# Optimization experiments

Hardware: AMD Instinct MI355X
Metric: run time of the kernel (lower is better)

## Reference

```python
import jax, jax.numpy as jnp
import numpy as np

N = 40000      # nodes
E = 640000     # edges (avg degree 16)
F = 128        # in_feats
OUT = 128      # out_feats


def setup_inputs() -> dict:
    key = jax.random.key(0)
    ks = jax.random.split(key, 8)
    feat = jax.random.normal(ks[0], (N, F), dtype=jnp.float32)
    src = jax.random.randint(ks[1], (E,), 0, N, dtype=jnp.int32)
    dst = jnp.sort(jax.random.randint(ks[2], (E,), 0, N, dtype=jnp.int32))
    # AttentionAGG: fc1 (2F -> F), fc2 (F -> 1); fc_layer (2F -> OUT)
    s1 = 1.0 / np.sqrt(2 * F)
    s2 = 1.0 / np.sqrt(F)
    w1 = jax.random.normal(ks[3], (2 * F, F), dtype=jnp.float32) * s1
    b1 = jnp.zeros((F,), dtype=jnp.float32)
    w2 = jax.random.normal(ks[4], (F, 1), dtype=jnp.float32) * s2
    b2 = jnp.zeros((1,), dtype=jnp.float32)
    wf = jax.random.normal(ks[5], (2 * F, OUT), dtype=jnp.float32) * s1
    bf = jnp.zeros((OUT,), dtype=jnp.float32)
    return {"feat": feat, "src": src, "dst": dst,
            "w1": w1, "b1": b1, "w2": w2, "b2": b2, "wf": wf, "bf": bf}


def reference(feat, src, dst, w1, b1, w2, b2, wf, bf):
    f = feat.shape[1]
    n = feat.shape[0]
    # fc1(concat(h_dst, m_src)) == h_dst @ w1[:F] + h_src @ w1[F:]  (edge_weight is None)
    proj_dst = feat @ w1[:f]          # [N, F]
    proj_src = feat @ w1[f:]          # [N, F]
    pre = jnp.tanh(proj_dst[dst] + proj_src[src] + b1)   # [E, F]
    scores = (pre @ w2)[:, 0] + b2[0]                    # [E]
    # softmax over the ragged incoming-edge set of each dst node
    smax = jax.ops.segment_max(scores, dst, num_segments=n, indices_are_sorted=True)
    ex = jnp.exp(scores - jax.lax.stop_gradient(smax)[dst])
    den = jax.ops.segment_sum(ex, dst, num_segments=n, indices_are_sorted=True)
    att = ex / den[dst]                                  # [E]
    # weighted segment-sum of messages (m_e = feat[src]); zero-degree nodes get 0
    neigh = jax.ops.segment_sum(att[:, None] * feat[src], dst,
                                num_segments=n, indices_are_sorted=True)  # [N, F]
    # fc_layer(concat(h_self, neigh))
    rst = feat @ wf[:f] + neigh @ wf[f:] + bf            # [N, OUT]
    return rst
```

## Files before the change

### kernel.cpp

```cpp
#include <hip/hip_runtime.h>
#include <math.h>

#define F 128
#define OUT 128

typedef unsigned short ushort_t;
typedef __attribute__((ext_vector_type(8))) short bfrag;
typedef __attribute__((ext_vector_type(4))) float ffrag;

union BU { unsigned u[4]; bfrag b; };

__device__ __forceinline__ float bf_lo(unsigned int u) {
    return __uint_as_float(u << 16);
}
__device__ __forceinline__ float bf_hi(unsigned int u) {
    return __uint_as_float(u & 0xffff0000u);
}
__device__ __forceinline__ ushort_t f2bf(float f) {
    unsigned int x = __float_as_uint(f);
    unsigned int r = x + 0x7fffu + ((x >> 16) & 1u);
    return (ushort_t)(r >> 16);
}
__device__ __forceinline__ unsigned pk2(float lo, float hi) {
    return (unsigned)f2bf(lo) | ((unsigned)f2bf(hi) << 16);
}

#define PSTRIDE 136
__global__ __launch_bounds__(256) void mega_kernel(
    const float* __restrict__ feat, const float* __restrict__ w1,
    const float* __restrict__ b1, const int* __restrict__ dst,
    int* __restrict__ row_ptr, ushort_t* __restrict__ e_dst,
    ushort_t* __restrict__ srcpack, ushort_t* __restrict__ abig,
    int n, int e, int nproj)
{
    if ((int)blockIdx.x >= nproj) {
        int i = ((int)blockIdx.x - nproj) * 256 + threadIdx.x;
        if (i >= e) return;
        int d = dst[i];
        int prev = (i == 0) ? -1 : dst[i - 1];
        for (int v = prev + 1; v <= d; ++v) row_ptr[v] = i;
        if (i == e - 1) {
            for (int v = d + 1; v <= n; ++v) row_ptr[v] = e;
        }
        return;
    }

    __shared__ ushort_t As[64 * PSTRIDE];
    const int t = threadIdx.x;
    const int wv = t >> 6, lane = t & 63;
    const int lm = lane & 15, quad = lane >> 4;
    const int row0 = blockIdx.x * 64;
    const int col0 = wv * 64;

    {
        const int r = t >> 2, q = t & 3;
        const int row = row0 + r;
        unsigned up[16];
        if (row < n) {
            const float* fp = feat + (size_t)row * F + 32 * q;
#pragma unroll
            for (int i4 = 0; i4 < 8; ++i4) {
                float4 a = *(const float4*)(fp + 4 * i4);
                up[2 * i4]     = pk2(a.x, a.y);
                up[2 * i4 + 1] = pk2(a.z, a.w);
            }
        } else {
#pragma unroll
            for (int i2 = 0; i2 < 16; ++i2) up[i2] = 0;
        }
#pragma unroll
        for (int i4 = 0; i4 < 4; ++i4)
            *(uint4*)(As + r * PSTRIDE + 32 * q + 8 * i4) =
                make_uint4(up[4 * i4], up[4 * i4 + 1], up[4 * i4 + 2], up[4 * i4 + 3]);
        if (row < n) {
#pragma unroll
            for (int i4 = 0; i4 < 4; ++i4)
                *(uint4*)(abig + (size_t)row * 256 + 32 * q + 8 * i4) =
                    make_uint4(up[4 * i4], up[4 * i4 + 1], up[4 * i4 + 2], up[4 * i4 + 3]);
#pragma unroll
            for (int i4 = 0; i4 < 8; ++i4)
                *(uint2*)(srcpack + (size_t)row * 256 + (8 * q + i4) * 8 + 4) =
                    make_uint2(up[2 * i4], up[2 * i4 + 1]);
        }
    }
    __syncthreads();

    ffrag acc[4][4];
#pragma unroll
    for (int mi = 0; mi < 4; ++mi)
#pragma unroll
        for (int ni = 0; ni < 4; ++ni) acc[mi][ni] = (ffrag){0.f, 0.f, 0.f, 0.f};

#pragma unroll
    for (int ks = 0; ks < 4; ++ks) {
        bfrag bfr[4];
#pragma unroll
        for (int ni = 0; ni < 4; ++ni) {
            const int jj = col0 + ni * 16 + lm;
            const float* wcol = (jj < F) ? (w1 + jj) : (w1 + (size_t)F * F + (jj - F));
            const int k0 = ks * 32 + quad * 8;
            BU bu;
#pragma unroll
            for (int l = 0; l < 4; ++l) {
                float x0 = wcol[(size_t)(k0 + 2 * l) * F];
                float x1 = wcol[(size_t)(k0 + 2 * l + 1) * F];
                bu.u[l] = pk2(x0, x1);
            }
            bfr[ni] = bu.b;
        }
#pragma unroll
        for (int mi = 0; mi < 4; ++mi) {
            bfrag af = *(const bfrag*)(As + (mi * 16 + lm) * PSTRIDE
                                       + ks * 32 + quad * 8);
#pragma unroll
            for (int ni = 0; ni < 4; ++ni)
                acc[mi][ni] = __builtin_amdgcn_mfma_f32_16x16x32_bf16(
                    af, bfr[ni], acc[mi][ni], 0, 0, 0);
        }
    }

#pragma unroll
    for (int ni = 0; ni < 4; ++ni) {
        const int j = col0 + ni * 16 + lm;
        const float bias = (j < F) ? b1[j] : 0.f;
#pragma unroll
        for (int mi = 0; mi < 4; ++mi) {
#pragma unroll
            for (int r = 0; r < 4; ++r) {
                int row = row0 + mi * 16 + quad * 4 + r;
                if (row >= n) continue;
                ushort_t ub = f2bf(__expf(2.f * (acc[mi][ni][r] + bias)));
                if (j < F) {
                    e_dst[(size_t)row * F + j] = ub;
                } else {
                    int f = j - F;
                    srcpack[(size_t)row * 256 + (f >> 2) * 8 + (f & 3)] = ub;
                }
            }
        }
    }
}

__global__ __launch_bounds__(256) void fused_kernel(
    const ushort_t* __restrict__ e_dst, const ushort_t* __restrict__ srcpack,
    const int* __restrict__ src, const int* __restrict__ row_ptr,
    const float* __restrict__ w2, ushort_t* __restrict__ abig, int n)
{
    const int v = (int)((blockIdx.x * 256u + threadIdx.x) >> 5);
    const int fl = threadIdx.x & 31;
    const int sbase = threadIdx.x & 32;

    const float4 wv4 = ((const float4*)w2)[fl];
    const float w0 = wv4.x, w1_ = wv4.y, w2_ = wv4.z, w3_ = wv4.w;
    float sw = w0 + w1_ + w2_ + w3_;
    float aw = fabsf(w0) + fabsf(w1_) + fabsf(w2_) + fabsf(w3_);
#pragma unroll
    for (int off = 16; off; off >>= 1) {
        sw += __shfl_xor(sw, off, 64);
        aw += __shfl_xor(aw, off, 64);
    }
    const float K = sw - aw;

    if (v >= n) return;
    const int begin = row_ptr[v], end = row_ptr[v + 1];

    const uint2 ud = *(const uint2*)(e_dst + (size_t)v * F + fl * 4);
    const float ea0 = bf_lo(ud.x), ea1 = bf_hi(ud.x);
    const float ea2 = bf_lo(ud.y), ea3 = bf_hi(ud.y);

    float s = 0.f, a0 = 0.f, a1 = 0.f, a2 = 0.f, a3 = 0.f;

    for (int cb = begin; cb < end; cb += 32) {
        const int clen = min(32, end - cb);
        const int sv = (fl < clen) ? src[cb + fl] : 0;
        int jj = 0;
        for (; jj + 4 <= clen; jj += 4) {
            uint4 u[4];
#pragma unroll
            for (int q = 0; q < 4; ++q) {
                const int sq = __shfl(sv, sbase + jj + q, 64);
                u[q] = ((const uint4*)(srcpack + (size_t)sq * 256))[fl];
            }
            float p[4];
#pragma unroll
            for (int q = 0; q < 4; ++q) {
                float r;
                r = __builtin_amdgcn_rcpf(fmaf(ea0, bf_lo(u[q].x), 1.f)); p[q] = w0 * r;
                r = __builtin_amdgcn_rcpf(fmaf(ea1, bf_hi(u[q].x), 1.f)); p[q] = fmaf(w1_, r, p[q]);
                r = __builtin_amdgcn_rcpf(fmaf(ea2, bf_lo(u[q].y), 1.f)); p[q] = fmaf(w2_, r, p[q]);
                r = __builtin_amdgcn_rcpf(fmaf(ea3, bf_hi(u[q].y), 1.f)); p[q] = fmaf(w3_, r, p[q]);
            }
#pragma unroll
            for (int off = 16; off; off >>= 1) {
#pragma unroll
                for (int q = 0; q < 4; ++q) p[q] += __shfl_xor(p[q], off, 64);
            }
            float g[4];
#pragma unroll
            for (int q = 0; q < 4; ++q) g[q] = __expf(fmaf(-2.f, p[q], K));
            s += (g[0] + g[1]) + (g[2] + g[3]);
#pragma unroll
            for (int q = 0; q < 4; ++q) {
                a0 = fmaf(g[q], bf_lo(u[q].z), a0);
                a1 = fmaf(g[q], bf_hi(u[q].z), a1);
                a2 = fmaf(g[q], bf_lo(u[q].w), a2);
                a3 = fmaf(g[q], bf_hi(u[q].w), a3);
            }
        }
        for (; jj < clen; ++jj) {
            const int s0 = __shfl(sv, sbase + jj, 64);
            const uint4 u0 = ((const uint4*)(srcpack + (size_t)s0 * 256))[fl];
            float r, p0;
            r = __builtin_amdgcn_rcpf(fmaf(ea0, bf_lo(u0.x), 1.f)); p0 = w0 * r;
            r = __builtin_amdgcn_rcpf(fmaf(ea1, bf_hi(u0.x), 1.f)); p0 = fmaf(w1_, r, p0);
            r = __builtin_amdgcn_rcpf(fmaf(ea2, bf_lo(u0.y), 1.f)); p0 = fmaf(w2_, r, p0);
            r = __builtin_amdgcn_rcpf(fmaf(ea3, bf_hi(u0.y), 1.f)); p0 = fmaf(w3_, r, p0);
#pragma unroll
            for (int off = 16; off; off >>= 1) p0 += __shfl_xor(p0, off, 64);
            const float g0 = __expf(fmaf(-2.f, p0, K));
            s += g0;
            a0 = fmaf(g0, bf_lo(u0.z), a0);
            a1 = fmaf(g0, bf_hi(u0.z), a1);
            a2 = fmaf(g0, bf_lo(u0.w), a2);
            a3 = fmaf(g0, bf_hi(u0.w), a3);
        }
    }

    const float inv = (end > begin) ? 1.f / s : 0.f;
    ushort4 o = make_ushort4(f2bf(a0 * inv), f2bf(a1 * inv),
                             f2bf(a2 * inv), f2bf(a3 * inv));
    *(ushort4*)(abig + (size_t)v * 256 + 128 + fl * 4) = o;
}

#define OSTRIDE 264
__global__ __launch_bounds__(256) void out_mfma_kernel(
    const ushort_t* __restrict__ abig, const float* __restrict__ wf,
    const float* __restrict__ bfv, float* __restrict__ out, int n)
{
    __shared__ ushort_t As[64 * OSTRIDE];
    const int t = threadIdx.x;
    const int wv = t >> 6, lane = t & 63;
    const int lm = lane & 15, quad = lane >> 4;
    const int row0 = blockIdx.x * 64;
    const int col0 = wv * 32;

    for (int i = t; i < 2048; i += 256) {
        int r = i >> 5, c8 = (i & 31) * 8;
        uint4 d = make_uint4(0, 0, 0, 0);
        if (row0 + r < n)
            d = *(const uint4*)(abig + (size_t)(row0 + r) * 256 + c8);
        *(uint4*)(As + r * OSTRIDE + c8) = d;
    }
    __syncthreads();

    ffrag acc[4][2];
#pragma unroll
    for (int mi = 0; mi < 4; ++mi)
#pragma unroll
        for (int ni = 0; ni < 2; ++ni) acc[mi][ni] = (ffrag){0.f, 0.f, 0.f, 0.f};

#pragma unroll
    for (int ks = 0; ks < 8; ++ks) {
        bfrag bfr[2];
#pragma unroll
        for (int ni = 0; ni < 2; ++ni) {
            const int jj = col0 + ni * 16 + lm;
            const int k0 = ks * 32 + quad * 8;
            BU bu;
#pragma unroll
            for (int l = 0; l < 4; ++l) {
                float x0 = wf[(size_t)(k0 + 2 * l) * F + jj];
                float x1 = wf[(size_t)(k0 + 2 * l + 1) * F + jj];
                bu.u[l] = pk2(x0, x1);
            }
            bfr[ni] = bu.b;
        }
#pragma unroll
        for (int mi = 0; mi < 4; ++mi) {
            bfrag af = *(const bfrag*)(As + (mi * 16 + lm) * OSTRIDE
                                       + ks * 32 + quad * 8);
#pragma unroll
            for (int ni = 0; ni < 2; ++ni)
                acc[mi][ni] = __builtin_amdgcn_mfma_f32_16x16x32_bf16(
                    af, bfr[ni], acc[mi][ni], 0, 0, 0);
        }
    }

#pragma unroll
    for (int ni = 0; ni < 2; ++ni) {
        const int j = col0 + ni * 16 + lm;
        const float bb = bfv[j];
#pragma unroll
        for (int mi = 0; mi < 4; ++mi) {
#pragma unroll
            for (int r = 0; r < 4; ++r) {
                int row = row0 + mi * 16 + quad * 4 + r;
                if (row < n) out[(size_t)row * OUT + j] = acc[mi][ni][r] + bb;
            }
        }
    }
}

extern "C" void kernel_launch(void* const* d_in, const int* in_sizes, int n_in,
                              void* d_out, int out_size, void* d_ws, size_t ws_size,
                              hipStream_t stream)
{
    const float* feat = (const float*)d_in[0];
    const int*   src  = (const int*)d_in[1];
    const int*   dst  = (const int*)d_in[2];
    const float* w1   = (const float*)d_in[3];
    const float* b1   = (const float*)d_in[4];
    const float* w2   = (const float*)d_in[5];
    const float* b2   = (const float*)d_in[6];  (void)b2;
    const float* wf   = (const float*)d_in[7];
    const float* bfv  = (const float*)d_in[8];
    float* out = (float*)d_out;

    const int n = in_sizes[0] / F;
    const int e = in_sizes[1];

    ushort_t* abig    = (ushort_t*)d_ws;
    ushort_t* e_dst   = abig + (size_t)n * 256;
    ushort_t* srcpack = e_dst + (size_t)n * 128;
    int* row_ptr      = (int*)(srcpack + (size_t)n * 256);

    const int nproj = (n + 63) / 64;
    const int nrp   = (e + 255) / 256;

    mega_kernel<<<nproj + nrp, 256, 0, stream>>>(
        feat, w1, b1, dst, row_ptr, e_dst, srcpack, abig, n, e, nproj);
    fused_kernel<<<(n + 7) / 8, 256, 0, stream>>>(
        e_dst, srcpack, src, row_ptr, w2, abig, n);
    out_mfma_kernel<<<(n + 63) / 64, 256, 0, stream>>>(abig, wf, bfv, out, n);
}
```

Measured before the change: 177.7 us.

## Pre-transpose weights to bf16 once and split projection GEMM into separate prep pass

Adds a prep kernel that converts feat to bf16, builds the packed source buffer, and writes w1 and wf transposed as bf16 so GEMM kernels can load B fragments with single vector loads instead of strided fp32 gathers plus conversion in every block. The projection GEMM now reads bf16 rows from the workspace and stages its epilogue through shared memory so e_dst and srcpack are written with wide coalesced stores instead of scattered 2-byte stores. The cost is an extra kernel launch and an extra global round-trip for the bf16 feature copy, which the projection GEMM previously produced in-register.

```diff
diff --git a/kernel.cpp b/kernel.cpp
--- a/kernel.cpp
+++ b/kernel.cpp
@@ -7,8 +7,6 @@
 typedef unsigned short ushort_t;
 typedef __attribute__((ext_vector_type(8))) short bfrag;
 typedef __attribute__((ext_vector_type(4))) float ffrag;
-
-union BU { unsigned u[4]; bfrag b; };
 
 __device__ __forceinline__ float bf_lo(unsigned int u) {
     return __uint_as_float(u << 16);
@@ -25,16 +23,37 @@
     return (unsigned)f2bf(lo) | ((unsigned)f2bf(hi) << 16);
 }
 
-#define PSTRIDE 136
-__global__ __launch_bounds__(256) void mega_kernel(
+__global__ __launch_bounds__(256) void prep_kernel(
     const float* __restrict__ feat, const float* __restrict__ w1,
-    const float* __restrict__ b1, const int* __restrict__ dst,
-    int* __restrict__ row_ptr, ushort_t* __restrict__ e_dst,
-    ushort_t* __restrict__ srcpack, ushort_t* __restrict__ abig,
-    int n, int e, int nproj)
-{
-    if ((int)blockIdx.x >= nproj) {
-        int i = ((int)blockIdx.x - nproj) * 256 + threadIdx.x;
+    const float* __restrict__ wf, const int* __restrict__ dst,
+    ushort_t* __restrict__ abig, ushort_t* __restrict__ srcpack,
+    ushort_t* __restrict__ btp, ushort_t* __restrict__ btf,
+    int* __restrict__ row_ptr, int n, int e, int nb0, int nb1, int nb2)
+{
+    const int b = blockIdx.x, t = threadIdx.x;
+    if (b < nb0) {
+        int i = b * 256 + t;
+        if (i >= n * 16) return;
+        int row = i >> 4, c = (i & 15) * 8;
+        float4 a = *(const float4*)(feat + (size_t)row * F + c);
+        float4 bb = *(const float4*)(feat + (size_t)row * F + c + 4);
+        unsigned p0 = pk2(a.x, a.y), p1 = pk2(a.z, a.w);
+        unsigned p2 = pk2(bb.x, bb.y), p3 = pk2(bb.z, bb.w);
+        *(uint4*)(abig + (size_t)row * 256 + c) = make_uint4(p0, p1, p2, p3);
+        *(uint2*)(srcpack + (size_t)row * 256 + c * 2 + 4) = make_uint2(p0, p1);
+        *(uint2*)(srcpack + (size_t)row * 256 + c * 2 + 12) = make_uint2(p2, p3);
+    } else if (b < nb0 + nb1) {
+        int idx = (b - nb0) * 256 + t;
+        int j = idx >> 7, k = idx & 127;
+        float v = (j < F) ? w1[(size_t)k * F + j]
+                          : w1[(size_t)(F + k) * F + (j - F)];
+        btp[idx] = f2bf(v);
+    } else if (b < nb0 + nb1 + nb2) {
+        int idx = (b - nb0 - nb1) * 256 + t;
+        int j = idx >> 8, k = idx & 255;
+        btf[idx] = f2bf(wf[(size_t)k * F + j]);
+    } else {
+        int i = (b - nb0 - nb1 - nb2) * 256 + t;
         if (i >= e) return;
         int d = dst[i];
         int prev = (i == 0) ? -1 : dst[i - 1];
@@ -42,49 +61,40 @@
         if (i == e - 1) {
             for (int v = d + 1; v <= n; ++v) row_ptr[v] = e;
         }
-        return;
-    }
-
-    __shared__ ushort_t As[64 * PSTRIDE];
+    }
+}
+
+#define PST 136
+__global__ __launch_bounds__(256) void proj_gemm_kernel(
+    const ushort_t* __restrict__ abig, const ushort_t* __restrict__ btp,
+    const float* __restrict__ b1, ushort_t* __restrict__ e_dst,
+    ushort_t* __restrict__ srcpack, int n)
+{
+    __shared__ ushort_t As[64 * PST];
+    __shared__ ushort_t Ep[4][16 * 80];
     const int t = threadIdx.x;
     const int wv = t >> 6, lane = t & 63;
     const int lm = lane & 15, quad = lane >> 4;
-    const int row0 = blockIdx.x * 64;
-    const int col0 = wv * 64;
-
-    {
-        const int r = t >> 2, q = t & 3;
-        const int row = row0 + r;
-        unsigned up[16];
-        if (row < n) {
-            const float* fp = feat + (size_t)row * F + 32 * q;
-#pragma unroll
-            for (int i4 = 0; i4 < 8; ++i4) {
-                float4 a = *(const float4*)(fp + 4 * i4);
-                up[2 * i4]     = pk2(a.x, a.y);
-                up[2 * i4 + 1] = pk2(a.z, a.w);
-            }
-        } else {
-#pragma unroll
-            for (int i2 = 0; i2 < 16; ++i2) up[i2] = 0;
-        }
-#pragma unroll
-        for (int i4 = 0; i4 < 4; ++i4)
-            *(uint4*)(As + r * PSTRIDE + 32 * q + 8 * i4) =
-                make_uint4(up[4 * i4], up[4 * i4 + 1], up[4 * i4 + 2], up[4 * i4 + 3]);
-        if (row < n) {
-#pragma unroll
-            for (int i4 = 0; i4 < 4; ++i4)
-                *(uint4*)(abig + (size_t)row * 256 + 32 * q + 8 * i4) =
-                    make_uint4(up[4 * i4], up[4 * i4 + 1], up[4 * i4 + 2], up[4 * i4 + 3]);
-#pragma unroll
-            for (int i4 = 0; i4 < 8; ++i4)
-                *(uint2*)(srcpack + (size_t)row * 256 + (8 * q + i4) * 8 + 4) =
-                    make_uint2(up[2 * i4], up[2 * i4 + 1]);
-        }
+    const int row0 = blockIdx.x * 64, col0 = wv * 64;
+
+#pragma unroll
+    for (int k = 0; k < 4; ++k) {
+        int l = k * 256 + t;
+        int r = l >> 4, ch = l & 15;
+        uint4 d = make_uint4(0, 0, 0, 0);
+        if (row0 + r < n) d = *(const uint4*)(abig + (size_t)(row0 + r) * 256 + ch * 8);
+        *(uint4*)(As + r * PST + ch * 8) = d;
     }
     __syncthreads();
 
+    bfrag bfr[4][4];
+#pragma unroll
+    for (int ks = 0; ks < 4; ++ks)
+#pragma unroll
+        for (int ni = 0; ni < 4; ++ni)
+            bfr[ks][ni] = *(const bfrag*)(btp + (size_t)(col0 + ni * 16 + lm) * 128
+                                          + ks * 32 + quad * 8);
+
     ffrag acc[4][4];
 #pragma unroll
     for (int mi = 0; mi < 4; ++mi)
@@ -92,49 +102,43 @@
         for (int ni = 0; ni < 4; ++ni) acc[mi][ni] = (ffrag){0.f, 0.f, 0.f, 0.f};
 
 #pragma unroll
-    for (int ks = 0; ks < 4; ++ks) {
-        bfrag bfr[4];
-#pragma unroll
-        for (int ni = 0; ni < 4; ++ni) {
-            const int jj = col0 + ni * 16 + lm;
-            const float* wcol = (jj < F) ? (w1 + jj) : (w1 + (size_t)F * F + (jj - F));
-            const int k0 = ks * 32 + quad * 8;
-            BU bu;
-#pragma unroll
-            for (int l = 0; l < 4; ++l) {
-                float x0 = wcol[(size_t)(k0 + 2 * l) * F];
-                float x1 = wcol[(size_t)(k0 + 2 * l + 1) * F];
-                bu.u[l] = pk2(x0, x1);
-            }
-            bfr[ni] = bu.b;
-        }
+    for (int ks = 0; ks < 4; ++ks)
 #pragma unroll
         for (int mi = 0; mi < 4; ++mi) {
-            bfrag af = *(const bfrag*)(As + (mi * 16 + lm) * PSTRIDE
-                                       + ks * 32 + quad * 8);
+            bfrag af = *(const bfrag*)(As + (mi * 16 + lm) * PST + ks * 32 + quad * 8);
 #pragma unroll
             for (int ni = 0; ni < 4; ++ni)
                 acc[mi][ni] = __builtin_amdgcn_mfma_f32_16x16x32_bf16(
-                    af, bfr[ni], acc[mi][ni], 0, 0, 0);
-        }
-    }
-
-#pragma unroll
-    for (int ni = 0; ni < 4; ++ni) {
-        const int j = col0 + ni * 16 + lm;
-        const float bias = (j < F) ? b1[j] : 0.f;
-#pragma unroll
-        for (int mi = 0; mi < 4; ++mi) {
-#pragma unroll
-            for (int r = 0; r < 4; ++r) {
-                int row = row0 + mi * 16 + quad * 4 + r;
-                if (row >= n) continue;
-                ushort_t ub = f2bf(__expf(2.f * (acc[mi][ni][r] + bias)));
-                if (j < F) {
-                    e_dst[(size_t)row * F + j] = ub;
+                    af, bfr[ks][ni], acc[mi][ni], 0, 0, 0);
+        }
+
+    float bias[4];
+#pragma unroll
+    for (int ni = 0; ni < 4; ++ni)
+        bias[ni] = (col0 < F) ? b1[col0 + ni * 16 + lm] : 0.f;
+
+#pragma unroll
+    for (int mi = 0; mi < 4; ++mi) {
+#pragma unroll
+        for (int ni = 0; ni < 4; ++ni)
+#pragma unroll
+            for (int r = 0; r < 4; ++r)
+                Ep[wv][(quad * 4 + r) * 80 + ni * 16 + lm] =
+                    f2bf(__expf(2.f * (acc[mi][ni][r] + bias[ni])));
+#pragma unroll
+        for (int ps = 0; ps < 2; ++ps) {
+            int rl = ps * 8 + (lane >> 3), co = (lane & 7) * 8;
+            uint4 vv = *(const uint4*)(&Ep[wv][rl * 80 + co]);
+            int grow = row0 + mi * 16 + rl;
+            if (grow < n) {
+                if (col0 < F) {
+                    *(uint4*)(e_dst + (size_t)grow * F + col0 + co) = vv;
                 } else {
-                    int f = j - F;
-                    srcpack[(size_t)row * 256 + (f >> 2) * 8 + (f & 3)] = ub;
+                    int f0 = col0 - F + co;
+                    *(uint2*)(srcpack + (size_t)grow * 256 + f0 * 2) =
+                        make_uint2(vv.x, vv.y);
+                    *(uint2*)(srcpack + (size_t)grow * 256 + f0 * 2 + 8) =
+                        make_uint2(vv.z, vv.w);
                 }
             }
         }
@@ -232,27 +236,35 @@
     *(ushort4*)(abig + (size_t)v * 256 + 128 + fl * 4) = o;
 }
 
-#define OSTRIDE 264
-__global__ __launch_bounds__(256) void out_mfma_kernel(
-    const ushort_t* __restrict__ abig, const float* __restrict__ wf,
+#define OST 280
+__global__ __launch_bounds__(256) void out_gemm_kernel(
+    const ushort_t* __restrict__ abig, const ushort_t* __restrict__ btf,
     const float* __restrict__ bfv, float* __restrict__ out, int n)
 {
-    __shared__ ushort_t As[64 * OSTRIDE];
+    __shared__ ushort_t As[64 * OST];
     const int t = threadIdx.x;
     const int wv = t >> 6, lane = t & 63;
     const int lm = lane & 15, quad = lane >> 4;
-    const int row0 = blockIdx.x * 64;
-    const int col0 = wv * 32;
-
-    for (int i = t; i < 2048; i += 256) {
-        int r = i >> 5, c8 = (i & 31) * 8;
+    const int row0 = blockIdx.x * 64, col0 = wv * 32;
+
+#pragma unroll
+    for (int k = 0; k < 8; ++k) {
+        int l = k * 256 + t;
+        int r = l >> 5, ch = l & 31;
         uint4 d = make_uint4(0, 0, 0, 0);
-        if (row0 + r < n)
-            d = *(const uint4*)(abig + (size_t)(row0 + r) * 256 + c8);
-        *(uint4*)(As + r * OSTRIDE + c8) = d;
+        if (row0 + r < n) d = *(const uint4*)(abig + (size_t)(row0 + r) * 256 + ch * 8);
+        *(uint4*)(As + r * OST + ch * 8) = d;
     }
     __syncthreads();
 
+    bfrag bfr[8][2];
+#pragma unroll
+    for (int ks = 0; ks < 8; ++ks)
+#pragma unroll
+        for (int ni = 0; ni < 2; ++ni)
+            bfr[ks][ni] = *(const bfrag*)(btf + (size_t)(col0 + ni * 16 + lm) * 256
+                                          + ks * 32 + quad * 8);
+
     ffrag acc[4][2];
 #pragma unroll
     for (int mi = 0; mi < 4; ++mi)
@@ -260,44 +272,27 @@
         for (int ni = 0; ni < 2; ++ni) acc[mi][ni] = (ffrag){0.f, 0.f, 0.f, 0.f};
 
 #pragma unroll
-    for (int ks = 0; ks < 8; ++ks) {
-        bfrag bfr[2];
-#pragma unroll
-        for (int ni = 0; ni < 2; ++ni) {
-            const int jj = col0 + ni * 16 + lm;
-            const int k0 = ks * 32 + quad * 8;
-            BU bu;
-#pragma unroll
-            for (int l = 0; l < 4; ++l) {
-                float x0 = wf[(size_t)(k0 + 2 * l) * F + jj];
-                float x1 = wf[(size_t)(k0 + 2 * l + 1) * F + jj];
-                bu.u[l] = pk2(x0, x1);
-            }
-            bfr[ni] = bu.b;
-        }
+    for (int ks = 0; ks < 8; ++ks)
 #pragma unroll
         for (int mi = 0; mi < 4; ++mi) {
-            bfrag af = *(const bfrag*)(As + (mi * 16 + lm) * OSTRIDE
-                                       + ks * 32 + quad * 8);
+            bfrag af = *(const bfrag*)(As + (mi * 16 + lm) * OST + ks * 32 + quad * 8);
 #pragma unroll
             for (int ni = 0; ni < 2; ++ni)
                 acc[mi][ni] = __builtin_amdgcn_mfma_f32_16x16x32_bf16(
-                    af, bfr[ni], acc[mi][ni], 0, 0, 0);
-        }
-    }
+                    af, bfr[ks][ni], acc[mi][ni], 0, 0, 0);
+        }
 
 #pragma unroll
     for (int ni = 0; ni < 2; ++ni) {
         const int j = col0 + ni * 16 + lm;
         const float bb = bfv[j];
 #pragma unroll
-        for (int mi = 0; mi < 4; ++mi) {
+        for (int mi = 0; mi < 4; ++mi)
 #pragma unroll
             for (int r = 0; r < 4; ++r) {
-                int row = row0 + mi * 16 + quad * 4 + r;
-                if (row < n) out[(size_t)row * OUT + j] = acc[mi][ni][r] + bb;
-            }
-        }
+                int grow = row0 + mi * 16 + quad * 4 + r;
+                if (grow < n) out[(size_t)grow * OUT + j] = acc[mi][ni][r] + bb;
+            }
     }
 }
 
@@ -322,14 +317,19 @@
     ushort_t* abig    = (ushort_t*)d_ws;
     ushort_t* e_dst   = abig + (size_t)n * 256;
     ushort_t* srcpack = e_dst + (size_t)n * 128;
-    int* row_ptr      = (int*)(srcpack + (size_t)n * 256);
-
-    const int nproj = (n + 63) / 64;
-    const int nrp   = (e + 255) / 256;
-
-    mega_kernel<<<nproj + nrp, 256, 0, stream>>>(
-        feat, w1, b1, dst, row_ptr, e_dst, srcpack, abig, n, e, nproj);
+    ushort_t* btp     = srcpack + (size_t)n * 256;
+    ushort_t* btf     = btp + 32768;
+    int* row_ptr      = (int*)(btf + 32768);
+
+    const int nb0 = (n * 16 + 255) / 256;
+    const int nb1 = 128, nb2 = 128;
+    const int nb3 = (e + 255) / 256;
+
+    prep_kernel<<<nb0 + nb1 + nb2 + nb3, 256, 0, stream>>>(
+        feat, w1, wf, dst, abig, srcpack, btp, btf, row_ptr, n, e, nb0, nb1, nb2);
+    proj_gemm_kernel<<<(n + 63) / 64, 256, 0, stream>>>(
+        abig, btp, b1, e_dst, srcpack, n);
     fused_kernel<<<(n + 7) / 8, 256, 0, stream>>>(
         e_dst, srcpack, src, row_ptr, w2, abig, n);
-    out_mfma_kernel<<<(n + 63) / 64, 256, 0, stream>>>(abig, wf, bfv, out, n);
-}
+    out_gemm_kernel<<<(n + 63) / 64, 256, 0, stream>>>(abig, btf, bfv, out, n);
+}
```

Measured after the change: 170.1 us. -4.3%, faster.

## Stage projection epilogue through LDS for coalesced stores; preload weight fragments

Applied to the files above, without the earlier changes.

In the projection kernel, the exp(2x) results are now staged per wave in a shared buffer and written as 16-byte rows to e_dst and srcpack, instead of scattered 2-byte stores. The srcpack feature half is interleaved from the LDS copy in the same store rather than in a separate pass. Both GEMM kernels now load all weight fragments into registers before the barrier, so the global weight reads overlap the A-tile staging. The output kernel's LDS stride also changes. The cost is more registers and shared memory per block, which may lower occupancy.

```diff
diff --git a/kernel.cpp b/kernel.cpp
--- a/kernel.cpp
+++ b/kernel.cpp
@@ -25,8 +25,8 @@
     return (unsigned)f2bf(lo) | ((unsigned)f2bf(hi) << 16);
 }
 
-#define PSTRIDE 136
-__global__ __launch_bounds__(256) void mega_kernel(
+#define PST 136
+__global__ __launch_bounds__(256) void k1_kernel(
     const float* __restrict__ feat, const float* __restrict__ w1,
     const float* __restrict__ b1, const int* __restrict__ dst,
     int* __restrict__ row_ptr, ushort_t* __restrict__ e_dst,
@@ -45,12 +45,12 @@
         return;
     }
 
-    __shared__ ushort_t As[64 * PSTRIDE];
+    __shared__ ushort_t As[64 * PST];
+    __shared__ ushort_t Ep[4][16 * 80];
     const int t = threadIdx.x;
     const int wv = t >> 6, lane = t & 63;
     const int lm = lane & 15, quad = lane >> 4;
-    const int row0 = blockIdx.x * 64;
-    const int col0 = wv * 64;
+    const int row0 = blockIdx.x * 64, col0 = wv * 64;
 
     {
         const int r = t >> 2, q = t & 3;
@@ -70,34 +70,24 @@
         }
 #pragma unroll
         for (int i4 = 0; i4 < 4; ++i4)
-            *(uint4*)(As + r * PSTRIDE + 32 * q + 8 * i4) =
+            *(uint4*)(As + r * PST + 32 * q + 8 * i4) =
                 make_uint4(up[4 * i4], up[4 * i4 + 1], up[4 * i4 + 2], up[4 * i4 + 3]);
         if (row < n) {
 #pragma unroll
             for (int i4 = 0; i4 < 4; ++i4)
                 *(uint4*)(abig + (size_t)row * 256 + 32 * q + 8 * i4) =
                     make_uint4(up[4 * i4], up[4 * i4 + 1], up[4 * i4 + 2], up[4 * i4 + 3]);
-#pragma unroll
-            for (int i4 = 0; i4 < 8; ++i4)
-                *(uint2*)(srcpack + (size_t)row * 256 + (8 * q + i4) * 8 + 4) =
-                    make_uint2(up[2 * i4], up[2 * i4 + 1]);
-        }
-    }
-    __syncthreads();
-
-    ffrag acc[4][4];
-#pragma unroll
-    for (int mi = 0; mi < 4; ++mi)
-#pragma unroll
-        for (int ni = 0; ni < 4; ++ni) acc[mi][ni] = (ffrag){0.f, 0.f, 0.f, 0.f};
-
-#pragma unroll
-    for (int ks = 0; ks < 4; ++ks) {
-        bfrag bfr[4];
+        }
+    }
+
+    bfrag bfr[4][4];
+#pragma unroll
+    for (int ks = 0; ks < 4; ++ks)
 #pragma unroll
         for (int ni = 0; ni < 4; ++ni) {
             const int jj = col0 + ni * 16 + lm;
-            const float* wcol = (jj < F) ? (w1 + jj) : (w1 + (size_t)F * F + (jj - F));
+            const float* wcol = (jj < F) ? (w1 + jj)
+                                         : (w1 + (size_t)F * F + (jj - F));
             const int k0 = ks * 32 + quad * 8;
             BU bu;
 #pragma unroll
@@ -106,36 +96,63 @@
                 float x1 = wcol[(size_t)(k0 + 2 * l + 1) * F];
                 bu.u[l] = pk2(x0, x1);
             }
-            bfr[ni] = bu.b;
-        }
+            bfr[ks][ni] = bu.b;
+        }
+    __syncthreads();
+
+    ffrag acc[4][4];
+#pragma unroll
+    for (int mi = 0; mi < 4; ++mi)
+#pragma unroll
+        for (int ni = 0; ni < 4; ++ni) acc[mi][ni] = (ffrag){0.f, 0.f, 0.f, 0.f};
+
+#pragma unroll
+    for (int ks = 0; ks < 4; ++ks)
 #pragma unroll
         for (int mi = 0; mi < 4; ++mi) {
-            bfrag af = *(const bfrag*)(As + (mi * 16 + lm) * PSTRIDE
-                                       + ks * 32 + quad * 8);
+            bfrag af = *(const bfrag*)(As + (mi * 16 + lm) * PST + ks * 32 + quad * 8);
 #pragma unroll
             for (int ni = 0; ni < 4; ++ni)
                 acc[mi][ni] = __builtin_amdgcn_mfma_f32_16x16x32_bf16(
-                    af, bfr[ni], acc[mi][ni], 0, 0, 0);
-        }
-    }
-
-#pragma unroll
-    for (int ni = 0; ni < 4; ++ni) {
-        const int j = col0 + ni * 16 + lm;
-        const float bias = (j < F) ? b1[j] : 0.f;
-#pragma unroll
-        for (int mi = 0; mi < 4; ++mi) {
-#pragma unroll
-            for (int r = 0; r < 4; ++r) {
-                int row = row0 + mi * 16 + quad * 4 + r;
-                if (row >= n) continue;
-                ushort_t ub = f2bf(__expf(2.f * (acc[mi][ni][r] + bias)));
-                if (j < F) {
-                    e_dst[(size_t)row * F + j] = ub;
-                } else {
-                    int f = j - F;
-                    srcpack[(size_t)row * 256 + (f >> 2) * 8 + (f & 3)] = ub;
-                }
+                    af, bfr[ks][ni], acc[mi][ni], 0, 0, 0);
+        }
+
+    float bias[4];
+#pragma unroll
+    for (int ni = 0; ni < 4; ++ni)
+        bias[ni] = (col0 < F) ? b1[col0 + ni * 16 + lm] : 0.f;
+
+#pragma unroll
+    for (int mi = 0; mi < 4; ++mi) {
+#pragma unroll
+        for (int ni = 0; ni < 4; ++ni)
+#pragma unroll
+            for (int r = 0; r < 4; ++r)
+                Ep[wv][(quad * 4 + r) * 80 + ni * 16 + lm] =
+                    f2bf(__expf(2.f * (acc[mi][ni][r] + bias[ni])));
+
+        if (col0 < F) {
+#pragma unroll
+            for (int ps = 0; ps < 2; ++ps) {
+                int rl = ps * 8 + (lane >> 3), co = (lane & 7) * 8;
+                uint4 vv = *(const uint4*)(&Ep[wv][rl * 80 + co]);
+                int grow = row0 + mi * 16 + rl;
+                if (grow < n)
+                    *(uint4*)(e_dst + (size_t)grow * F + col0 + co) = vv;
+            }
+        } else {
+            const int cbase = (col0 - F) >> 2;
+#pragma unroll
+            for (int ps = 0; ps < 4; ++ps) {
+                int rl = ps * 4 + (lane >> 4);
+                int c  = lane & 15;
+                int cg = cbase + c;
+                uint2 es = *(const uint2*)(&Ep[wv][rl * 80 + c * 4]);
+                uint2 ft = *(const uint2*)(As + (mi * 16 + rl) * PST + cg * 4);
+                int grow = row0 + mi * 16 + rl;
+                if (grow < n)
+                    *(uint4*)(srcpack + (size_t)grow * 256 + cg * 8) =
+                        make_uint4(es.x, es.y, ft.x, ft.y);
             }
         }
     }
@@ -232,36 +249,29 @@
     *(ushort4*)(abig + (size_t)v * 256 + 128 + fl * 4) = o;
 }
 
-#define OSTRIDE 264
-__global__ __launch_bounds__(256) void out_mfma_kernel(
+#define OST 280
+__global__ __launch_bounds__(256) void out_gemm_kernel(
     const ushort_t* __restrict__ abig, const float* __restrict__ wf,
     const float* __restrict__ bfv, float* __restrict__ out, int n)
 {
-    __shared__ ushort_t As[64 * OSTRIDE];
+    __shared__ ushort_t As[64 * OST];
     const int t = threadIdx.x;
     const int wv = t >> 6, lane = t & 63;
     const int lm = lane & 15, quad = lane >> 4;
-    const int row0 = blockIdx.x * 64;
-    const int col0 = wv * 32;
-
-    for (int i = t; i < 2048; i += 256) {
-        int r = i >> 5, c8 = (i & 31) * 8;
+    const int row0 = blockIdx.x * 64, col0 = wv * 32;
+
+#pragma unroll
+    for (int k = 0; k < 8; ++k) {
+        int l = k * 256 + t;
+        int r = l >> 5, ch = l & 31;
         uint4 d = make_uint4(0, 0, 0, 0);
-        if (row0 + r < n)
-            d = *(const uint4*)(abig + (size_t)(row0 + r) * 256 + c8);
-        *(uint4*)(As + r * OSTRIDE + c8) = d;
-    }
-    __syncthreads();
-
-    ffrag acc[4][2];
-#pragma unroll
-    for (int mi = 0; mi < 4; ++mi)
-#pragma unroll
-        for (int ni = 0; ni < 2; ++ni) acc[mi][ni] = (ffrag){0.f, 0.f, 0.f, 0.f};
-
-#pragma unroll
-    for (int ks = 0; ks < 8; ++ks) {
-        bfrag bfr[2];
+        if (row0 + r < n) d = *(const uint4*)(abig + (size_t)(row0 + r) * 256 + ch * 8);
+        *(uint4*)(As + r * OST + ch * 8) = d;
+    }
+
+    bfrag bfr[8][2];
+#pragma unroll
+    for (int ks = 0; ks < 8; ++ks)
 #pragma unroll
         for (int ni = 0; ni < 2; ++ni) {
             const int jj = col0 + ni * 16 + lm;
@@ -273,31 +283,38 @@
                 float x1 = wf[(size_t)(k0 + 2 * l + 1) * F + jj];
                 bu.u[l] = pk2(x0, x1);
             }
-            bfr[ni] = bu.b;
-        }
+            bfr[ks][ni] = bu.b;
+        }
+    __syncthreads();
+
+    ffrag acc[4][2];
+#pragma unroll
+    for (int mi = 0; mi < 4; ++mi)
+#pragma unroll
+        for (int ni = 0; ni < 2; ++ni) acc[mi][ni] = (ffrag){0.f, 0.f, 0.f, 0.f};
+
+#pragma unroll
+    for (int ks = 0; ks < 8; ++ks)
 #pragma unroll
         for (int mi = 0; mi < 4; ++mi) {
-            bfrag af = *(const bfrag*)(As + (mi * 16 + lm) * OSTRIDE
-                                       + ks * 32 + quad * 8);
+            bfrag af = *(const bfrag*)(As + (mi * 16 + lm) * OST + ks * 32 + quad * 8);
 #pragma unroll
             for (int ni = 0; ni < 2; ++ni)
                 acc[mi][ni] = __builtin_amdgcn_mfma_f32_16x16x32_bf16(
-                    af, bfr[ni], acc[mi][ni], 0, 0, 0);
-        }
-    }
+                    af, bfr[ks][ni], acc[mi][ni], 0, 0, 0);
+        }
 
 #pragma unroll
     for (int ni = 0; ni < 2; ++ni) {
         const int j = col0 + ni * 16 + lm;
         const float bb = bfv[j];
 #pragma unroll
-        for (int mi = 0; mi < 4; ++mi) {
+        for (int mi = 0; mi < 4; ++mi)
 #pragma unroll
             for (int r = 0; r < 4; ++r) {
-                int row = row0 + mi * 16 + quad * 4 + r;
-                if (row < n) out[(size_t)row * OUT + j] = acc[mi][ni][r] + bb;
-            }
-        }
+                int grow = row0 + mi * 16 + quad * 4 + r;
+                if (grow < n) out[(size_t)grow * OUT + j] = acc[mi][ni][r] + bb;
+            }
     }
 }
 
@@ -327,9 +344,9 @@
     const int nproj = (n + 63) / 64;
     const int nrp   = (e + 255) / 256;
 
-    mega_kernel<<<nproj + nrp, 256, 0, stream>>>(
+    k1_kernel<<<nproj + nrp, 256, 0, stream>>>(
         feat, w1, b1, dst, row_ptr, e_dst, srcpack, abig, n, e, nproj);
     fused_kernel<<<(n + 7) / 8, 256, 0, stream>>>(
         e_dst, srcpack, src, row_ptr, w2, abig, n);
-    out_mfma_kernel<<<(n + 63) / 64, 256, 0, stream>>>(abig, wf, bfv, out, n);
-}
+    out_gemm_kernel<<<(n + 63) / 64, 256, 0, stream>>>(abig, wf, bfv, out, n);
+}
```

After: 189.3 us. +6.5%, slower.
